# Kernel optimization log

Hardware: AMD Instinct MI355X
Metric: run time of the kernel (lower is better)

Reference implementation:

```python
import jax, jax.numpy as jnp
import numpy as np

# HopfBifur activation is not provided in the source. The cell calls
# self.activation(new_state, new_state**2). We implement the Hopf-normal-form
# radial map r * (mu - r^2) with mu=1, i.e. act(r, r2) = r * (1 - r2).

def hopf_bifur(r, r2):
    return r * (1.0 - r2)


def setup_inputs() -> dict:
    key = jax.random.key(0)
    k1, k2, k3 = jax.random.split(key, 3)
    B, T, D = 128, 2048, 128
    x = jax.random.normal(k1, (B, T, D), dtype=jnp.float32)
    kernel = jax.random.normal(k2, (D, D), dtype=jnp.float32) / np.sqrt(D)
    recurrent_kernel = jax.random.normal(k3, (D, D), dtype=jnp.float32) / np.sqrt(D)
    return {"x": x, "kernel": kernel, "recurrent_kernel": recurrent_kernel}


def reference(x, kernel, recurrent_kernel):
    # x: [B, T, D]; sequential recurrence over T via lax.scan.
    B, T, D = x.shape
    # Precompute input projection for all timesteps at once (same math,
    # just hoists the time-independent matmul out of the loop).
    kern_map = jnp.einsum('btd,de->bte', x, kernel)  # [B, T, D]

    def step(state, km_t):
        # new_state = sqrt(cos(x_t @ K)^2 + sin(s_{t-1} @ R)^2)
        rec_map = state @ recurrent_kernel
        new_state = jnp.sqrt(jnp.cos(km_t) ** 2 + jnp.sin(rec_map) ** 2)
        out = hopf_bifur(new_state, new_state ** 2)
        return new_state, out

    s0 = jnp.zeros((B, D), dtype=x.dtype)
    _, outs = jax.lax.scan(step, s0, jnp.swapaxes(kern_map, 0, 1))  # [T, B, D]
    return jnp.swapaxes(outs, 0, 1)  # [B, T, D]
```

## Files before the change

kernel.cpp:

```cpp
#include <hip/hip_runtime.h>
#include <math.h>


constexpr int Bb = 128;
constexpr int Tt = 2048;
constexpr int Dd = 128;
constexpr int PP_ROWS = 128;
constexpr int GROUP = 16;

__global__ __launch_bounds__(256, 2)
void pratt_prepass(const float* __restrict__ x,
                   const float* __restrict__ Kmat,
                   float* __restrict__ kmT)
{
    __shared__ float Ks[Dd][Dd];
    {
        const float4* Kg  = reinterpret_cast<const float4*>(Kmat);
        float4*       KsV = reinterpret_cast<float4*>(&Ks[0][0]);
#pragma unroll
        for (int j = 0; j < 16; ++j)
            KsV[threadIdx.x + j * 256] = Kg[threadIdx.x + j * 256];
    }
    __syncthreads();

    const int  rgrp = threadIdx.x >> 4;
    const int  cgrp = threadIdx.x & 15;
    const int  c0   = cgrp << 3;
    const long row0 = (long)blockIdx.x * PP_ROWS + (long)rgrp * 8;

    const float4* xr[8];
#pragma unroll
    for (int r = 0; r < 8; ++r)
        xr[r] = reinterpret_cast<const float4*>(x + (size_t)(row0 + r) * Dd);

    float acc[8][8];
#pragma unroll
    for (int r = 0; r < 8; ++r)
#pragma unroll
        for (int c = 0; c < 8; ++c) acc[r][c] = 0.f;

    for (int k4 = 0; k4 < Dd / 4; ++k4) {
        float4 xq[8];
#pragma unroll
        for (int r = 0; r < 8; ++r) xq[r] = xr[r][k4];
        float4 kf[4][2];
#pragma unroll
        for (int kk = 0; kk < 4; ++kk) {
            const float* krow = &Ks[k4 * 4 + kk][c0];
            kf[kk][0] = *reinterpret_cast<const float4*>(krow);
            kf[kk][1] = *reinterpret_cast<const float4*>(krow + 4);
        }
#pragma unroll
        for (int kk = 0; kk < 4; ++kk) {
#pragma unroll
            for (int r = 0; r < 8; ++r) {
                const float xv = (kk == 0) ? xq[r].x : (kk == 1) ? xq[r].y
                               : (kk == 2) ? xq[r].z : xq[r].w;
                acc[r][0] = fmaf(xv, kf[kk][0].x, acc[r][0]);
                acc[r][1] = fmaf(xv, kf[kk][0].y, acc[r][1]);
                acc[r][2] = fmaf(xv, kf[kk][0].z, acc[r][2]);
                acc[r][3] = fmaf(xv, kf[kk][0].w, acc[r][3]);
                acc[r][4] = fmaf(xv, kf[kk][1].x, acc[r][4]);
                acc[r][5] = fmaf(xv, kf[kk][1].y, acc[r][5]);
                acc[r][6] = fmaf(xv, kf[kk][1].z, acc[r][6]);
                acc[r][7] = fmaf(xv, kf[kk][1].w, acc[r][7]);
            }
        }
    }

    const int b   = blockIdx.x >> 4;
    const int t00 = (blockIdx.x & 15) * PP_ROWS + rgrp * 8;
#pragma unroll
    for (int c = 0; c < 8; ++c) {
        float* p = kmT + ((size_t)b * Dd + (c0 + c)) * Tt + t00;
        *reinterpret_cast<float4*>(p)     = make_float4(acc[0][c], acc[1][c], acc[2][c], acc[3][c]);
        *reinterpret_cast<float4*>(p + 4) = make_float4(acc[4][c], acc[5][c], acc[6][c], acc[7][c]);
    }
}

__global__ __launch_bounds__(512, 1)
void pratt_rnn(const float* __restrict__ kmT,
               const float* __restrict__ Rmat,
               float* __restrict__ out)
{
    const int tid = threadIdx.x;
    const int d   = tid >> 2;
    const int kq  = tid & 3;
    const int k0  = kq << 5;
    const int rot = kq << 1;

    float Rr[32];
#pragma unroll
    for (int ii = 0; ii < 8; ++ii) {
        const int c = (ii + rot) & 7;
#pragma unroll
        for (int j = 0; j < 4; ++j)
            Rr[4*ii + j] = Rmat[(k0 + 4*c + j) * Dd + d];
    }

    __shared__ float sbuf[2][Dd];
    if (tid < Dd) sbuf[0][tid] = 0.0f;
    __syncthreads();

    const float* kmd = kmT + ((size_t)blockIdx.x * Dd + d) * Tt;
    float*       ob  = out + (size_t)blockIdx.x * Tt * Dd;

    float4 cur0 = *reinterpret_cast<const float4*>(kmd + 0);
    float4 cur1 = *reinterpret_cast<const float4*>(kmd + 4);
    float4 cur2 = *reinterpret_cast<const float4*>(kmd + 8);
    float4 cur3 = *reinterpret_cast<const float4*>(kmd + 12);

    for (int g = 0; g < Tt / GROUP; ++g) {
        const int gn = (g + 1 < Tt / GROUP) ? g + 1 : g;
        const float* pn = kmd + (size_t)gn * GROUP;
        const float4 nx0 = *reinterpret_cast<const float4*>(pn + 0);
        const float4 nx1 = *reinterpret_cast<const float4*>(pn + 4);
        const float4 nx2 = *reinterpret_cast<const float4*>(pn + 8);
        const float4 nx3 = *reinterpret_cast<const float4*>(pn + 12);

        float ovals[GROUP];
        const int tbase = g * GROUP;

#pragma unroll
        for (int j = 0; j < GROUP; ++j) {
            const float4 qs  = (j < 4) ? cur0 : (j < 8) ? cur1 : (j < 12) ? cur2 : cur3;
            const int    jm  = j & 3;
            const float  kmv = (jm == 0) ? qs.x : (jm == 1) ? qs.y : (jm == 2) ? qs.z : qs.w;
            const int    rb  = j & 1;

            float ra0=0.f, ra1=0.f, ra2=0.f, ra3=0.f;
#pragma unroll
            for (int ii = 0; ii < 8; ++ii) {
                const int c = (ii + rot) & 7;
                const float4 sv = *reinterpret_cast<const float4*>(&sbuf[rb][k0 + 4*c]);
                ra0 = fmaf(sv.x, Rr[4*ii+0], ra0);
                ra1 = fmaf(sv.y, Rr[4*ii+1], ra1);
                ra2 = fmaf(sv.z, Rr[4*ii+2], ra2);
                ra3 = fmaf(sv.w, Rr[4*ii+3], ra3);
            }
            float rc = (ra0 + ra1) + (ra2 + ra3);
            rc += __shfl_xor(rc, 1);
            rc += __shfl_xor(rc, 2);

            const float cc = __cosf(kmv);
            const float ss = __sinf(rc);
            const float ns = __builtin_amdgcn_sqrtf(fmaf(cc, cc, ss * ss));
            ovals[j] = ns * (1.0f - ns * ns);

            if (kq == 0) sbuf[rb ^ 1][d] = ns;
            __syncthreads();
        }

        if (kq == 1) {
#pragma unroll
            for (int j = 0; j < GROUP; ++j)
                ob[(size_t)(tbase + j) * Dd + d] = ovals[j];
        }

        cur0 = nx0; cur1 = nx1; cur2 = nx2; cur3 = nx3;
    }
}

__global__ __launch_bounds__(512, 2)
void pratt_fused(const float* __restrict__ x,
                 const float* __restrict__ Kmat,
                 const float* __restrict__ Rmat,
                 float* __restrict__ out)
{
    const int b   = blockIdx.x;
    const int tid = threadIdx.x;
    const int d   = tid >> 2;
    const int kq  = tid & 3;
    const int k0  = kq << 5;

    float Kr[32], Rr[32];
#pragma unroll
    for (int i = 0; i < 32; ++i) {
        Kr[i] = Kmat[(k0 + i) * Dd + d];
        Rr[i] = Rmat[(k0 + i) * Dd + d];
    }
    __shared__ float sbuf[2][Dd];
    if (tid < Dd) sbuf[0][tid] = 0.0f;
    __syncthreads();

    const float* xb = x   + (size_t)b * Tt * Dd;
    float*       ob = out + (size_t)b * Tt * Dd;
    int cur = 0;
    for (int t = 0; t < Tt; ++t) {
        const float4* xr = reinterpret_cast<const float4*>(xb + (size_t)t * Dd) + (k0 >> 2);
        const float4* s4 = reinterpret_cast<const float4*>(&sbuf[cur][k0]);
        float ka = 0.f, ra = 0.f;
#pragma unroll
        for (int i = 0; i < 8; ++i) {
            const float4 xv = xr[i];
            const float4 sv = s4[i];
            ka = fmaf(xv.x, Kr[4*i+0], ka); ka = fmaf(xv.y, Kr[4*i+1], ka);
            ka = fmaf(xv.z, Kr[4*i+2], ka); ka = fmaf(xv.w, Kr[4*i+3], ka);
            ra = fmaf(sv.x, Rr[4*i+0], ra); ra = fmaf(sv.y, Rr[4*i+1], ra);
            ra = fmaf(sv.z, Rr[4*i+2], ra); ra = fmaf(sv.w, Rr[4*i+3], ra);
        }
        ka += __shfl_xor(ka, 1); ka += __shfl_xor(ka, 2);
        ra += __shfl_xor(ra, 1); ra += __shfl_xor(ra, 2);
        const float cc = cosf(ka), ss = sinf(ra);
        const float ns = sqrtf(fmaf(cc, cc, ss * ss));
        const float o  = ns * (1.0f - ns * ns);
        const int nxt = cur ^ 1;
        if (kq == 0) sbuf[nxt][d] = ns;
        if (kq == 1) ob[(size_t)t * Dd + d] = o;
        __syncthreads();
        cur = nxt;
    }
}

extern "C" void kernel_launch(void* const* d_in, const int* in_sizes, int n_in,
                              void* d_out, int out_size, void* d_ws, size_t ws_size,
                              hipStream_t stream)
{
    const float* x = (const float*)d_in[0];
    const float* K = (const float*)d_in[1];
    const float* R = (const float*)d_in[2];
    float* out = (float*)d_out;

    const size_t km_bytes = (size_t)Bb * Tt * Dd * sizeof(float);
    if (ws_size >= km_bytes) {
        float* kmT = (float*)d_ws;
        pratt_prepass<<<dim3(Bb * Tt / PP_ROWS), dim3(256), 0, stream>>>(x, K, kmT);
        pratt_rnn<<<dim3(Bb), dim3(512), 0, stream>>>(kmT, R, out);
    } else {
        pratt_fused<<<dim3(Bb), dim3(512), 0, stream>>>(x, K, R, out);
    }
}
```

Before: 1.056 ms.

## Use one thread per output column in recurrent kernel, dropping shuffle reduction

Result: slower. 1.818 ms (+72.1%).

```diff
diff --git a/kernel.cpp b/kernel.cpp
--- a/kernel.cpp
+++ b/kernel.cpp
@@ -78,28 +78,19 @@
     }
 }
 
-__global__ __launch_bounds__(512, 1)
+__global__ __launch_bounds__(128)
 void pratt_rnn(const float* __restrict__ kmT,
                const float* __restrict__ Rmat,
                float* __restrict__ out)
 {
-    const int tid = threadIdx.x;
-    const int d   = tid >> 2;
-    const int kq  = tid & 3;
-    const int k0  = kq << 5;
-    const int rot = kq << 1;
-
-    float Rr[32];
-#pragma unroll
-    for (int ii = 0; ii < 8; ++ii) {
-        const int c = (ii + rot) & 7;
-#pragma unroll
-        for (int j = 0; j < 4; ++j)
-            Rr[4*ii + j] = Rmat[(k0 + 4*c + j) * Dd + d];
-    }
-
-    __shared__ float sbuf[2][Dd];
-    if (tid < Dd) sbuf[0][tid] = 0.0f;
+    const int d = threadIdx.x;
+
+    float Rr[Dd];
+#pragma unroll
+    for (int k = 0; k < Dd; ++k) Rr[k] = Rmat[k * Dd + d];
+
+    __shared__ __align__(16) float sbuf[2][Dd];
+    sbuf[0][d] = 0.0f;
     __syncthreads();
 
     const float* kmd = kmT + ((size_t)blockIdx.x * Dd + d) * Tt;
@@ -128,34 +119,34 @@
             const float  kmv = (jm == 0) ? qs.x : (jm == 1) ? qs.y : (jm == 2) ? qs.z : qs.w;
             const int    rb  = j & 1;
 
-            float ra0=0.f, ra1=0.f, ra2=0.f, ra3=0.f;
-#pragma unroll
-            for (int ii = 0; ii < 8; ++ii) {
-                const int c = (ii + rot) & 7;
-                const float4 sv = *reinterpret_cast<const float4*>(&sbuf[rb][k0 + 4*c]);
-                ra0 = fmaf(sv.x, Rr[4*ii+0], ra0);
-                ra1 = fmaf(sv.y, Rr[4*ii+1], ra1);
-                ra2 = fmaf(sv.z, Rr[4*ii+2], ra2);
-                ra3 = fmaf(sv.w, Rr[4*ii+3], ra3);
+            const float4* sv4 = reinterpret_cast<const float4*>(&sbuf[rb][0]);
+            float acc[8];
+#pragma unroll
+            for (int a = 0; a < 8; ++a) acc[a] = 0.f;
+#pragma unroll
+            for (int k4 = 0; k4 < Dd / 4; ++k4) {
+                const float4 sv = sv4[k4];
+                const int a = k4 & 7;
+                acc[a] = fmaf(sv.x, Rr[4*k4+0], acc[a]);
+                acc[a] = fmaf(sv.y, Rr[4*k4+1], acc[a]);
+                acc[a] = fmaf(sv.z, Rr[4*k4+2], acc[a]);
+                acc[a] = fmaf(sv.w, Rr[4*k4+3], acc[a]);
             }
-            float rc = (ra0 + ra1) + (ra2 + ra3);
-            rc += __shfl_xor(rc, 1);
-            rc += __shfl_xor(rc, 2);
+            const float rc = ((acc[0] + acc[1]) + (acc[2] + acc[3]))
+                           + ((acc[4] + acc[5]) + (acc[6] + acc[7]));
 
             const float cc = __cosf(kmv);
             const float ss = __sinf(rc);
             const float ns = __builtin_amdgcn_sqrtf(fmaf(cc, cc, ss * ss));
             ovals[j] = ns * (1.0f - ns * ns);
 
-            if (kq == 0) sbuf[rb ^ 1][d] = ns;
+            sbuf[rb ^ 1][d] = ns;
             __syncthreads();
         }
 
-        if (kq == 1) {
-#pragma unroll
-            for (int j = 0; j < GROUP; ++j)
-                ob[(size_t)(tbase + j) * Dd + d] = ovals[j];
-        }
+#pragma unroll
+        for (int j = 0; j < GROUP; ++j)
+            ob[(size_t)(tbase + j) * Dd + d] = ovals[j];
 
         cur0 = nx0; cur1 = nx1; cur2 = nx2; cur3 = nx3;
     }
@@ -225,7 +216,7 @@
     if (ws_size >= km_bytes) {
         float* kmT = (float*)d_ws;
         pratt_prepass<<<dim3(Bb * Tt / PP_ROWS), dim3(256), 0, stream>>>(x, K, kmT);
-        pratt_rnn<<<dim3(Bb), dim3(512), 0, stream>>>(kmT, R, out);
+        pratt_rnn<<<dim3(Bb), dim3(128), 0, stream>>>(kmT, R, out);
     } else {
         pratt_fused<<<dim3(Bb), dim3(512), 0, stream>>>(x, K, R, out);
     }
```
